# Performance work log

Hardware: AMD Instinct MI355X
Metric: run time of the kernel (lower is better)

Reference implementation:

```python
import jax, jax.numpy as jnp
import numpy as np

N, E, D = 50000, 800000, 64  # nodes, edges, hidden (in_hid == out_hid, n_heads == 1)


def setup_inputs() -> dict:
    key = jax.random.key(0)
    ks = jax.random.split(key, 12)

    def lin(k, out_d, in_d):
        k1, k2 = jax.random.split(k)
        s = 1.0 / np.sqrt(in_d)
        W = jax.random.uniform(k1, (out_d, in_d), minval=-s, maxval=s, dtype=jnp.float32)
        b = jax.random.uniform(k2, (out_d,), minval=-s, maxval=s, dtype=jnp.float32)
        return W, b

    Wt, bt = lin(ks[0], D, D + 1)   # w_transfer: Linear(d_input+1, d_k)
    Wq, bq = lin(ks[1], D, D)
    Wks, bks = lin(ks[2], D, D)
    Wkd, bkd = lin(ks[3], D, D)
    Wvs, bvs = lin(ks[4], D, D)
    Wvd, bvd = lin(ks[5], D, D)
    return {
        "x": jax.random.normal(ks[6], (N, D), dtype=jnp.float32),
        "edge_index": jax.random.randint(ks[7], (2, E), 0, N),
        "edge_time": jax.random.uniform(ks[8], (E,), dtype=jnp.float32),
        "x_time": jax.random.uniform(ks[9], (N,), dtype=jnp.float32),
        "edge_same": jax.random.randint(ks[10], (E,), 0, 2).astype(jnp.float32),
        "ln_gamma": jnp.ones((D,), jnp.float32),
        "ln_beta": jnp.zeros((D,), jnp.float32),
        "Wt": Wt, "bt": bt, "Wq": Wq, "bq": bq,
        "Wks": Wks, "bks": bks, "Wkd": Wkd, "bkd": bkd,
        "Wvs": Wvs, "bvs": bvs, "Wvd": Wvd, "bvd": bvd,
    }


def _gelu(x):
    return jax.nn.gelu(x, approximate=False)  # torch F.gelu default (erf)


def _temporal_enc(t):
    # TemporalEncoding: div_term[j] = 1/10000^(2*(j//2)/D); sin on even cols, cos on odd
    j = jnp.arange(D)
    div = 1.0 / jnp.power(jnp.float32(10000.0), (2.0 * (j // 2)).astype(jnp.float32) / D)
    pe = (t.reshape(-1, 1) * 200.0) * div[None, :]  # [E, D]
    return jnp.where((j % 2 == 0)[None, :], jnp.sin(pe), jnp.cos(pe))


def reference(x, edge_index, edge_time, x_time, edge_same, ln_gamma, ln_beta,
              Wt, bt, Wq, bq, Wks, bks, Wkd, bkd, Wvs, bvs, Wvd, bvd):
    residual = x
    # LayerNorm(d_input)
    mu = jnp.mean(x, axis=-1, keepdims=True)
    var = jnp.var(x, axis=-1, keepdims=True)
    xn = (x - mu) / jnp.sqrt(var + 1e-5) * ln_gamma + ln_beta

    src, dst = edge_index[0], edge_index[1]  # x_j = source, x_i = target (PyG default)
    x_j = xn[src]                            # [E, D] gather
    x_i = xn[dst]                            # [E, D] gather
    es = edge_same.reshape(-1, 1)            # [E, 1]

    te = _temporal_enc(edge_time)            # [E, D]
    xt = _gelu(jnp.concatenate([x_j, edge_time.reshape(-1, 1)], axis=1) @ Wt.T + bt) + te

    q = x_i @ Wq.T + bq
    k = es * (xt @ Wks.T + bks) + (1.0 - es) * (xt @ Wkd.T + bkd)
    att = jnp.sum(k * q, axis=-1) / jnp.sqrt(jnp.float32(D))  # [E]

    # PyG-style segment softmax over edges sharing the same receiver
    m = jax.ops.segment_max(att, dst, num_segments=N)
    m = jnp.where(jnp.isfinite(m), m, 0.0)
    ex = jnp.exp(att - m[dst])
    denom = jax.ops.segment_sum(ex, dst, num_segments=N)
    attn = ex / (denom[dst] + 1e-16)         # [E]

    v = es * (xt @ Wvs.T + bvs) + (1.0 - es) * (xt @ Wvd.T + bvd)
    aggr = jax.ops.segment_sum(attn[:, None] * v, dst, num_segments=N)  # [N, D]

    return residual + _gelu(aggr)            # dropout is identity in eval
```

## Files before the change

kernel.cpp:

```cpp
#include <hip/hip_runtime.h>
#include <hip/hip_bf16.h>
#include <math.h>

#define D 64

typedef __attribute__((ext_vector_type(8))) short bf16x8;
typedef __attribute__((ext_vector_type(8))) _Float16 f16x8;
typedef __attribute__((ext_vector_type(8))) unsigned short u16x8;
typedef __attribute__((ext_vector_type(4))) float f32x4;
typedef unsigned short u16;

__device__ __forceinline__ float gelu_erf(float x) {
    return 0.5f * x * (1.0f + erff(x * 0.70710678118654752f));
}
__device__ __forceinline__ float gelu_fast(float x) {
    float t = x * fmaf(x * x, -0.1029432f, -2.3022080f);
    float e = __builtin_amdgcn_exp2f(t);
    return x * __builtin_amdgcn_rcpf(1.0f + e);
}
__device__ __forceinline__ u16 f2bf(float v) {
    __hip_bfloat16 h = __float2bfloat16(v);
    return *(u16*)&h;
}
__device__ __forceinline__ float bf2f(u16 v) {
    return __uint_as_float(((unsigned int)v) << 16);
}
__device__ __forceinline__ u16 f2h(float v) {
    _Float16 h = (_Float16)v;
    return __builtin_bit_cast(u16, h);
}
__device__ __forceinline__ void atomic_pk_add_f16(u16* addr, float lo, float hi) {
    unsigned int p = (unsigned int)f2h(lo) | ((unsigned int)f2h(hi) << 16);
    asm volatile("global_atomic_pk_add_f16 %0, %1, off sc1" :: "v"(addr), "v"(p));
}
__device__ __forceinline__ int pi_perm(int p) { return ((p & 3) << 4) | (p >> 2); }

__device__ __forceinline__ float rowsum16(float v) {
    int x;
    x = __builtin_amdgcn_update_dpp(0, __builtin_bit_cast(int, v), 0xB1, 0xF, 0xF, true);
    v += __builtin_bit_cast(float, x);
    x = __builtin_amdgcn_update_dpp(0, __builtin_bit_cast(int, v), 0x4E, 0xF, 0xF, true);
    v += __builtin_bit_cast(float, x);
    x = __builtin_amdgcn_update_dpp(0, __builtin_bit_cast(int, v), 0x141, 0xF, 0xF, true);
    v += __builtin_bit_cast(float, x);
    x = __builtin_amdgcn_update_dpp(0, __builtin_bit_cast(int, v), 0x140, 0xF, 0xF, true);
    v += __builtin_bit_cast(float, x);
    return v;
}

__global__ __launch_bounds__(256) void prep_hist(
    const float* __restrict__ Wt, const float* __restrict__ Wq,
    const float* __restrict__ Wks, const float* __restrict__ Wkd,
    const float* __restrict__ Wvs, const float* __restrict__ Wvd,
    u16* __restrict__ WtB, u16* __restrict__ WqB,
    u16* __restrict__ WksB, u16* __restrict__ WkdB,
    u16* __restrict__ WvsB, u16* __restrict__ WvdB,
    const int* __restrict__ ei, const float* __restrict__ esame,
    int* __restrict__ cnt, int* __restrict__ rank, int E)
{
    if (blockIdx.x < 12) {
        int task = blockIdx.x * 4 + (threadIdx.x >> 6);
        int lane = threadIdx.x & 63;
        int wsel = task >> 3, f = task & 7;
        int c = lane & 15, quad = lane >> 4;
        int nt = f >> 1, kk = f & 1;
        for (int j = 0; j < 8; ++j) {
            int n = nt * 16 + c, k = kk * 32 + quad * 8 + j;
            float v; u16* dp; bool h16 = false;
            switch (wsel) {
                case 0: v = Wt[n * 65 + k];  dp = WtB;  break;
                case 1: v = Wq[n * 64 + k];  dp = WqB;  break;
                case 2: v = Wks[k * 64 + n]; dp = WksB; break;
                case 3: v = Wkd[k * 64 + n]; dp = WkdB; break;
                case 4: v = Wvs[n * 64 + pi_perm(k)]; dp = WvsB; h16 = true; break;
                default: v = Wvd[n * 64 + pi_perm(k)]; dp = WvdB; h16 = true; break;
            }
            dp[(f * 64 + lane) * 8 + j] = h16 ? f2h(v) : f2bf(v);
        }
    } else {
        int gid = (blockIdx.x - 12) * 256 + threadIdx.x;
        int stride = (gridDim.x - 12) * 256;
        int e[4]; bool v[4]; int key[4];
        #pragma unroll
        for (int j = 0; j < 4; ++j) { e[j] = gid + j * stride; v[j] = e[j] < E; }
        #pragma unroll
        for (int j = 0; j < 4; ++j) {
            if (v[j]) key[j] = 2 * ei[E + e[j]] + (esame[e[j]] > 0.5f ? 0 : 1);
        }
        int r[4];
        #pragma unroll
        for (int j = 0; j < 4; ++j) {
            if (v[j]) r[j] = atomicAdd(&cnt[key[j]], 1);
        }
        #pragma unroll
        for (int j = 0; j < 4; ++j) {
            if (v[j]) rank[e[j]] = r[j];
        }
    }
}

#define SCAN_CHUNK 2048

__global__ __launch_bounds__(256) void scan_phaseA(const int* __restrict__ cnt,
                                                   int* __restrict__ bsum, int M)
{
    int base = blockIdx.x * SCAN_CHUNK;
    int s = 0;
    for (int i = threadIdx.x; i < SCAN_CHUNK; i += 256) {
        int idx = base + i;
        s += (idx < M) ? cnt[idx] : 0;
    }
    #pragma unroll
    for (int o = 32; o; o >>= 1) s += __shfl_xor(s, o);
    __shared__ int red[4];
    if ((threadIdx.x & 63) == 0) red[threadIdx.x >> 6] = s;
    __syncthreads();
    if (threadIdx.x == 0) bsum[blockIdx.x] = red[0] + red[1] + red[2] + red[3];
}

__global__ __launch_bounds__(256) void scan_phaseC(const int* __restrict__ cnt,
                                                   const int* __restrict__ bsum,
                                                   int* __restrict__ cursor, int M)
{
    __shared__ int wsum[4];
    __shared__ int sboff;
    if (threadIdx.x < 64) {
        int v = ((int)threadIdx.x < (int)blockIdx.x) ? bsum[threadIdx.x] : 0;
        #pragma unroll
        for (int o = 32; o; o >>= 1) v += __shfl_xor(v, o);
        if (threadIdx.x == 0) sboff = v;
    }
    int base = blockIdx.x * SCAN_CHUNK;
    int i0 = base + threadIdx.x * 8;
    int vals[8];
    int tsum = 0;
    #pragma unroll
    for (int j = 0; j < 8; ++j) {
        int idx = i0 + j;
        vals[j] = (idx < M) ? cnt[idx] : 0;
        tsum += vals[j];
    }
    int lane = threadIdx.x & 63;
    int w = threadIdx.x >> 6;
    int inc = tsum;
    #pragma unroll
    for (int o = 1; o < 64; o <<= 1) {
        int v = __shfl_up(inc, o);
        if (lane >= o) inc += v;
    }
    if (lane == 63) wsum[w] = inc;
    __syncthreads();
    int woff = 0;
    #pragma unroll
    for (int k = 0; k < 4; ++k) woff += (k < w) ? wsum[k] : 0;
    int excl = woff + (inc - tsum) + sboff;
    #pragma unroll
    for (int j = 0; j < 8; ++j) {
        int idx = i0 + j;
        if (idx < M) cursor[idx] = excl;
        excl += vals[j];
    }
}

__global__ __launch_bounds__(256) void scatter_qgemm(
    const int* __restrict__ ei, const float* __restrict__ et,
    const float* __restrict__ esame, const int* __restrict__ cursor,
    const int* __restrict__ rank,
    int4* __restrict__ evk, int E, int GS,
    const float* __restrict__ x, const float* __restrict__ gamma, const float* __restrict__ beta,
    const u16* __restrict__ WqB, const u16* __restrict__ WksB, const u16* __restrict__ WkdB,
    const float* __restrict__ bq, const float* __restrict__ bks, const float* __restrict__ bkd,
    u16* __restrict__ xnb, u16* __restrict__ qk2, float* __restrict__ bq2, int N)
{
    __shared__ u16 qtile[4][16 * 64];
    __shared__ u16 stile[4][32 * 64];

    if (blockIdx.x < GS) {
        int gid = blockIdx.x * 256 + threadIdx.x;
        int stride = GS * 256;
        int e[4]; bool v[4]; int key[4]; int rk[4]; int src[4]; float tv[4];
        #pragma unroll
        for (int j = 0; j < 4; ++j) { e[j] = gid + j * stride; v[j] = e[j] < E; }
        #pragma unroll
        for (int j = 0; j < 4; ++j) {
            if (v[j]) {
                key[j] = 2 * ei[E + e[j]] + (esame[e[j]] > 0.5f ? 0 : 1);
                rk[j] = rank[e[j]];
                src[j] = ei[e[j]];
                tv[j] = et[e[j]];
            }
        }
        int pos[4];
        #pragma unroll
        for (int j = 0; j < 4; ++j) {
            if (v[j]) pos[j] = cursor[key[j]] + rk[j];
        }
        #pragma unroll
        for (int j = 0; j < 4; ++j) {
            if (v[j]) evk[pos[j]] = make_int4(key[j], __float_as_int(tv[j]), src[j], 0);
        }
        return;
    }

    const int lane = threadIdx.x & 63;
    const int c = lane & 15, quad = lane >> 4;
    const int w = threadIdx.x >> 6;
    const int wave = (blockIdx.x - GS) * 4 + w;
    const int n0r = wave * 16;
    const bool active = n0r < N;
    const int n0 = active ? n0r : 0;
    const int rowA = (n0 + c < N) ? n0 + c : N - 1;

    const float* xrow = x + (long)rowA * D;
    f32x4 xa = *(const f32x4*)(xrow + quad * 8);
    f32x4 xb = *(const f32x4*)(xrow + quad * 8 + 4);
    f32x4 xc = *(const f32x4*)(xrow + 32 + quad * 8);
    f32x4 xd = *(const f32x4*)(xrow + 32 + quad * 8 + 4);
    float s = 0.f, s2 = 0.f;
    #pragma unroll
    for (int j = 0; j < 4; ++j) {
        s += xa[j] + xb[j] + xc[j] + xd[j];
        s2 += xa[j] * xa[j] + xb[j] * xb[j] + xc[j] * xc[j] + xd[j] * xd[j];
    }
    s += __shfl_xor(s, 16);  s += __shfl_xor(s, 32);
    s2 += __shfl_xor(s2, 16); s2 += __shfl_xor(s2, 32);
    float mu = s * (1.0f / 64.0f);
    float var = s2 * (1.0f / 64.0f) - mu * mu;
    float rinv = rsqrtf(var + 1e-5f);
    f32x4 ga = *(const f32x4*)(gamma + quad * 8);
    f32x4 gb = *(const f32x4*)(gamma + quad * 8 + 4);
    f32x4 gc = *(const f32x4*)(gamma + 32 + quad * 8);
    f32x4 gd = *(const f32x4*)(gamma + 32 + quad * 8 + 4);
    f32x4 ba = *(const f32x4*)(beta + quad * 8);
    f32x4 bb = *(const f32x4*)(beta + quad * 8 + 4);
    f32x4 bc = *(const f32x4*)(beta + 32 + quad * 8);
    f32x4 bd = *(const f32x4*)(beta + 32 + quad * 8 + 4);
    bf16x8 a0, a1;
    #pragma unroll
    for (int j = 0; j < 4; ++j) {
        a0[j]     = (short)f2bf(fmaf((xa[j] - mu) * rinv, ga[j], ba[j]));
        a0[4 + j] = (short)f2bf(fmaf((xb[j] - mu) * rinv, gb[j], bb[j]));
        a1[j]     = (short)f2bf(fmaf((xc[j] - mu) * rinv, gc[j], bc[j]));
        a1[4 + j] = (short)f2bf(fmaf((xd[j] - mu) * rinv, gd[j], bd[j]));
    }
    *(bf16x8*)(xnb + (long)rowA * D + quad * 8) = a0;
    *(bf16x8*)(xnb + (long)rowA * D + 32 + quad * 8) = a1;

    float bqc[4], bksc[4], bkdc[4];
    #pragma unroll
    for (int t = 0; t < 4; ++t) {
        bqc[t] = bq[t * 16 + c]; bksc[t] = bks[t * 16 + c]; bkdc[t] = bkd[t * 16 + c];
    }

    f32x4 accq[4];
    #pragma unroll
    for (int t = 0; t < 4; ++t) {
        bf16x8 b0 = *(const bf16x8*)(WqB + ((t * 2 + 0) * 64 + lane) * 8);
        bf16x8 b1 = *(const bf16x8*)(WqB + ((t * 2 + 1) * 64 + lane) * 8);
        f32x4 z = {0.f, 0.f, 0.f, 0.f};
        z = __builtin_amdgcn_mfma_f32_16x16x32_bf16(a0, b0, z, 0, 0, 0);
        z = __builtin_amdgcn_mfma_f32_16x16x32_bf16(a1, b1, z, 0, 0, 0);
        accq[t] = z;
    }
    #pragma unroll
    for (int r = 0; r < 4; ++r) {
        float qv[4], ss = 0.f, sd = 0.f;
        #pragma unroll
        for (int t = 0; t < 4; ++t) {
            qv[t] = accq[t][r] + bqc[t];
            ss = fmaf(qv[t], bksc[t], ss);
            sd = fmaf(qv[t], bkdc[t], sd);
        }
        #pragma unroll
        for (int o = 1; o < 16; o <<= 1) { ss += __shfl_xor(ss, o); sd += __shfl_xor(sd, o); }
        int nrow = n0 + quad * 4 + r;
        if (active && c == 0 && nrow < N)
            *(float2*)(bq2 + 2 * nrow) = make_float2(ss, sd);
        #pragma unroll
        for (int t = 0; t < 4; ++t)
            qtile[w][(quad * 4 + r) * 64 + t * 16 + c] = f2bf(qv[t]);
    }
    __syncthreads();

    const u16* qrow = &qtile[w][c * 64 + quad * 8];
    bf16x8 q0 = *(const bf16x8*)(qrow);
    bf16x8 q1 = *(const bf16x8*)(qrow + 32);
    #pragma unroll
    for (int t = 0; t < 4; ++t) {
        bf16x8 bs0 = *(const bf16x8*)(WksB + ((t * 2 + 0) * 64 + lane) * 8);
        bf16x8 bs1 = *(const bf16x8*)(WksB + ((t * 2 + 1) * 64 + lane) * 8);
        bf16x8 bd0 = *(const bf16x8*)(WkdB + ((t * 2 + 0) * 64 + lane) * 8);
        bf16x8 bd1 = *(const bf16x8*)(WkdB + ((t * 2 + 1) * 64 + lane) * 8);
        f32x4 zs = {0.f, 0.f, 0.f, 0.f}, zd = {0.f, 0.f, 0.f, 0.f};
        zs = __builtin_amdgcn_mfma_f32_16x16x32_bf16(q0, bs0, zs, 0, 0, 0);
        zs = __builtin_amdgcn_mfma_f32_16x16x32_bf16(q1, bs1, zs, 0, 0, 0);
        zd = __builtin_amdgcn_mfma_f32_16x16x32_bf16(q0, bd0, zd, 0, 0, 0);
        zd = __builtin_amdgcn_mfma_f32_16x16x32_bf16(q1, bd1, zd, 0, 0, 0);
        #pragma unroll
        for (int r = 0; r < 4; ++r) {
            int m = quad * 4 + r;
            stile[w][(2 * m + 0) * 64 + c * 4 + t] = f2bf(zs[r]);
            stile[w][(2 * m + 1) * 64 + c * 4 + t] = f2bf(zd[r]);
        }
    }
    __syncthreads();
    if (active) {
        int nrows = min(16, N - n0);
        const u16x8* sp = (const u16x8*)&stile[w][0];
        u16x8* dp = (u16x8*)(qk2 + (long)(2 * n0) * D);
        int cnt8 = nrows * 16;
        for (int j = lane; j < cnt8; j += 64) dp[j] = sp[j];
    }
}

template<bool FULL>
__device__ __forceinline__ void edge_run(
    const int4* __restrict__ evk, const u16* __restrict__ xnb,
    const bf16x8* bfrag, const float* btc, const float* w64c,
    const float* dvr, float phr,
    const u16* __restrict__ qk2, const float* __restrict__ bq2,
    u16* __restrict__ A, float* __restrict__ den,
    int base, int end, int qchunk, int c, int quad)
{
    const float S = 0.18033688011f;
    int cur_key = -1;
    float racc0 = 0.f, racc1 = 0.f, racc2 = 0.f, racc3 = 0.f, rden = 0.f;
    ushort4 q4 = {0, 0, 0, 0};
    float bqv = 0.f;

    const int rowbase = base + (c >> 2) * qchunk + (c & 3);
    const int qbase   = base + quad * qchunk;
    const int last    = end - 1;

    int srcC = ((const int*)(evk + (FULL ? rowbase : min(rowbase, last))))[2];

    for (int i = 0; i < qchunk; i += 4) {
        const u16* ar = xnb + srcC * D + quad * 8;
        bf16x8 a0 = *(const bf16x8*)(ar);
        bf16x8 a1 = *(const bf16x8*)(ar + 32);

        srcC = ((const int*)(evk + min(rowbase + i + 4, last)))[2];

        int qb = qbase + i;
        int2 kt0 = *(const int2*)(evk + (FULL ? qb     : min(qb,     last)));
        int2 kt1 = *(const int2*)(evk + (FULL ? qb + 1 : min(qb + 1, last)));
        int2 kt2 = *(const int2*)(evk + (FULL ? qb + 2 : min(qb + 2, last)));
        int2 kt3 = *(const int2*)(evk + (FULL ? qb + 3 : min(qb + 3, last)));

        f32x4 acc[4];
        #pragma unroll
        for (int t = 0; t < 4; ++t) {
            f32x4 z = {0.f, 0.f, 0.f, 0.f};
            z = __builtin_amdgcn_mfma_f32_16x16x32_bf16(a0, bfrag[t * 2 + 0], z, 0, 0, 0);
            z = __builtin_amdgcn_mfma_f32_16x16x32_bf16(a1, bfrag[t * 2 + 1], z, 0, 0, 0);
            acc[t] = z;
        }

        #pragma unroll
        for (int r = 0; r < 4; ++r) {
            int2 kt = (r == 0) ? kt0 : (r == 1) ? kt1 : (r == 2) ? kt2 : kt3;
            int keym = kt.x;
            float tm = __int_as_float(kt.y);

            if (keym != cur_key) {
                ushort4 nq = *(const ushort4*)(qk2 + keym * D + c * 4);
                float nb = bq2[keym];
                if (cur_key >= 0) {
                    u16* ap = A + cur_key * D + c * 4;
                    atomic_pk_add_f16(ap, racc0, racc1);
                    atomic_pk_add_f16(ap + 2, racc2, racc3);
                    if (c == 0) atomicAdd(&den[cur_key], rden);
                }
                cur_key = keym;
                q4 = nq;
                bqv = nb * S;
                racc0 = racc1 = racc2 = racc3 = 0.f;
                rden = 0.f;
            }

            float x0 = acc[0][r] + fmaf(tm, w64c[0], btc[0]);
            float x1 = acc[1][r] + fmaf(tm, w64c[1], btc[1]);
            float x2 = acc[2][r] + fmaf(tm, w64c[2], btc[2]);
            float x3 = acc[3][r] + fmaf(tm, w64c[3], btc[3]);
            float v0 = gelu_fast(x0) + __builtin_amdgcn_sinf(fmaf(tm, dvr[0], phr));
            float v1 = gelu_fast(x1) + __builtin_amdgcn_sinf(fmaf(tm, dvr[1], phr));
            float v2 = gelu_fast(x2) + __builtin_amdgcn_sinf(fmaf(tm, dvr[2], phr));
            float v3 = gelu_fast(x3) + __builtin_amdgcn_sinf(fmaf(tm, dvr[3], phr));

            float p = v0 * bf2f(q4.x);
            p = fmaf(v1, bf2f(q4.y), p);
            p = fmaf(v2, bf2f(q4.z), p);
            p = fmaf(v3, bf2f(q4.w), p);
            p = rowsum16(p);

            float ex = __builtin_amdgcn_exp2f(fmaf(p, S, bqv));
            if (!FULL && (qbase + i + r >= end)) ex = 0.f;

            racc0 = fmaf(ex, v0, racc0);
            racc1 = fmaf(ex, v1, racc1);
            racc2 = fmaf(ex, v2, racc2);
            racc3 = fmaf(ex, v3, racc3);
            rden += ex;
        }
    }

    if (cur_key >= 0) {
        u16* ap = A + cur_key * D + c * 4;
        atomic_pk_add_f16(ap, racc0, racc1);
        atomic_pk_add_f16(ap + 2, racc2, racc3);
        if (c == 0) atomicAdd(&den[cur_key], rden);
    }
}

__global__ __launch_bounds__(256) void edge_pass(
    const int4* __restrict__ evk, const u16* __restrict__ xnb, const u16* __restrict__ WtB,
    const float* __restrict__ Wt, const float* __restrict__ bt,
    const u16* __restrict__ qk2, const float* __restrict__ bq2,
    u16* __restrict__ A, float* __restrict__ den, int E, int chunk)
{
    const int lane = threadIdx.x & 63;
    const int c = lane & 15, quad = lane >> 4;
    const int wave = blockIdx.x * 4 + (threadIdx.x >> 6);
    const int base = wave * chunk;
    if (base >= E) return;
    const int end = min(base + chunk, E);
    const int qchunk = chunk >> 2;

    bf16x8 bfrag[8];
    #pragma unroll
    for (int f = 0; f < 8; ++f)
        bfrag[f] = *(const bf16x8*)(WtB + (f * 64 + lane) * 8);

    float btc[4], w64c[4], dvr[4];
    #pragma unroll
    for (int t = 0; t < 4; ++t) {
        int dim = t * 16 + c;
        btc[t] = bt[dim];
        w64c[t] = Wt[dim * 65 + 64];
        dvr[t] = 31.830988618f * expf(-9.210340371976184f * (float)(2 * (dim >> 1)) * (1.0f / 64.0f));
    }
    const float phr = (c & 1) ? 0.25f : 0.0f;

    if (base + chunk <= E)
        edge_run<true>(evk, xnb, bfrag, btc, w64c, dvr, phr, qk2, bq2, A, den,
                       base, end, qchunk, c, quad);
    else
        edge_run<false>(evk, xnb, bfrag, btc, w64c, dvr, phr, qk2, bq2, A, den,
                        base, end, qchunk, c, quad);
}

__global__ __launch_bounds__(256) void vgemm(
    const float* __restrict__ x, const u16* __restrict__ A, const float* __restrict__ den,
    const u16* __restrict__ WvsB, const u16* __restrict__ WvdB,
    const float* __restrict__ bvs, const float* __restrict__ bvd,
    float* __restrict__ out, int N)
{
    const int lane = threadIdx.x & 63;
    const int c = lane & 15, quad = lane >> 4;
    const int wave = blockIdx.x * 4 + (threadIdx.x >> 6);
    const int n0 = wave * 16;
    if (n0 >= N) return;
    const int rowA = (n0 + c < N) ? n0 + c : N - 1;

    float bvsc[4], bvdc[4];
    #pragma unroll
    for (int t = 0; t < 4; ++t) { bvsc[t] = bvs[t * 16 + c]; bvdc[t] = bvd[t * 16 + c]; }

    const u16* srow = A + (long)(2 * rowA) * D + quad * 8;
    const u16* drow = A + (long)(2 * rowA + 1) * D + quad * 8;
    f16x8 s0 = *(const f16x8*)(srow);
    f16x8 s1 = *(const f16x8*)(srow + 32);
    f16x8 d0 = *(const f16x8*)(drow);
    f16x8 d1 = *(const f16x8*)(drow + 32);

    f32x4 oacc[4];
    #pragma unroll
    for (int t = 0; t < 4; ++t) {
        f16x8 bs0 = *(const f16x8*)(WvsB + ((t * 2 + 0) * 64 + lane) * 8);
        f16x8 bs1 = *(const f16x8*)(WvsB + ((t * 2 + 1) * 64 + lane) * 8);
        f16x8 bd0 = *(const f16x8*)(WvdB + ((t * 2 + 0) * 64 + lane) * 8);
        f16x8 bd1 = *(const f16x8*)(WvdB + ((t * 2 + 1) * 64 + lane) * 8);
        f32x4 z = {0.f, 0.f, 0.f, 0.f};
        z = __builtin_amdgcn_mfma_f32_16x16x32_f16(s0, bs0, z, 0, 0, 0);
        z = __builtin_amdgcn_mfma_f32_16x16x32_f16(s1, bs1, z, 0, 0, 0);
        z = __builtin_amdgcn_mfma_f32_16x16x32_f16(d0, bd0, z, 0, 0, 0);
        z = __builtin_amdgcn_mfma_f32_16x16x32_f16(d1, bd1, z, 0, 0, 0);
        oacc[t] = z;
    }

    #pragma unroll
    for (int r = 0; r < 4; ++r) {
        int n = n0 + quad * 4 + r;
        if (n >= N) continue;
        float ds = den[2 * n], dd = den[2 * n + 1];
        float inv = 1.0f / (ds + dd + 1e-16f);
        float fs = ds * inv, fd = dd * inv;
        #pragma unroll
        for (int t = 0; t < 4; ++t) {
            long idx = (long)n * D + t * 16 + c;
            float o = fmaf(oacc[t][r], inv, fmaf(fs, bvsc[t], fd * bvdc[t]));
            out[idx] = x[idx] + gelu_erf(o);
        }
    }
}

extern "C" void kernel_launch(void* const* d_in, const int* in_sizes, int n_in,
                              void* d_out, int out_size, void* d_ws, size_t ws_size,
                              hipStream_t stream) {
    const float* x        = (const float*)d_in[0];
    const int*   ei       = (const int*)d_in[1];
    const float* et       = (const float*)d_in[2];
    const float* esame    = (const float*)d_in[4];
    const float* ln_gamma = (const float*)d_in[5];
    const float* ln_beta  = (const float*)d_in[6];
    const float* Wt  = (const float*)d_in[7];
    const float* bt  = (const float*)d_in[8];
    const float* Wq  = (const float*)d_in[9];
    const float* bq  = (const float*)d_in[10];
    const float* Wks = (const float*)d_in[11];
    const float* bks = (const float*)d_in[12];
    const float* Wkd = (const float*)d_in[13];
    const float* bkd = (const float*)d_in[14];
    const float* Wvs = (const float*)d_in[15];
    const float* bvs = (const float*)d_in[16];
    const float* Wvd = (const float*)d_in[17];
    const float* bvd = (const float*)d_in[18];
    float* out = (float*)d_out;

    const int N = in_sizes[0] / D;
    const int E = in_sizes[2];
    const int M = 2 * N;

    u16* A      = (u16*)d_ws;
    float* den  = (float*)(A + (long)M * D);
    int* cnt    = (int*)(den + M);
    int* cursor = cnt + M;
    float* bq2  = (float*)(cursor + M);
    int4* evk   = (int4*)(bq2 + M);
    int* bsum   = (int*)(evk + E);
    u16* xnb    = (u16*)(bsum + 256);
    u16* qk2    = xnb + (long)N * D;
    u16* WtB    = qk2 + (long)M * D;
    u16* WqB    = WtB + 4096;
    u16* WksB   = WqB + 4096;
    u16* WkdB   = WksB + 4096;
    u16* WvsB   = WkdB + 4096;
    u16* WvdB   = WvsB + 4096;
    int* rank   = (int*)A;
    const size_t rankBytes = (size_t)E * 4;

    hipMemsetAsync((char*)A + rankBytes, 0,
                   ((size_t)M * D * 2 - rankBytes) + (size_t)M * 4 * 2, stream);

    const int GH = (E + 256 * 4 - 1) / (256 * 4);
    prep_hist<<<12 + GH, 256, 0, stream>>>(Wt, Wq, Wks, Wkd, Wvs, Wvd,
                                           WtB, WqB, WksB, WkdB, WvsB, WvdB,
                                           ei, esame, cnt, rank, E);
    const int nbScan = (M + SCAN_CHUNK - 1) / SCAN_CHUNK;
    scan_phaseA<<<nbScan, 256, 0, stream>>>(cnt, bsum, M);
    scan_phaseC<<<nbScan, 256, 0, stream>>>(cnt, bsum, cursor, M);

    const int GS = (E + 256 * 4 - 1) / (256 * 4);
    const int GQ = ((N + 15) / 16 + 3) / 4;
    scatter_qgemm<<<GS + GQ, 256, 0, stream>>>(
        ei, et, esame, cursor, rank, evk, E, GS,
        x, ln_gamma, ln_beta, WqB, WksB, WkdB, bq, bks, bkd,
        xnb, qk2, bq2, N);

    hipMemsetAsync(A, 0, rankBytes, stream);

    const int nwaves = 2048 * 4;
    const int chunk = ((E + nwaves * 16 - 1) / (nwaves * 16)) * 16;
    edge_pass<<<2048, 256, 0, stream>>>(evk, xnb, WtB, Wt, bt,
                                        qk2, bq2, A, den, E, chunk);
    vgemm<<<GQ, 256, 0, stream>>>(x, A, den, WvsB, WvdB, bvs, bvd, out, N);
}
```

Measured before the change: 236.2 us.

## Move Wt fragments to LDS, defer segment atomics, drop extra rank memset

The edge pass now stages the Wt bf16 fragments in shared memory and reads them from LDS on every iteration, where it previously kept them in registers. The goal is to free VGPRs and allow higher occupancy. Finished segment results are stashed as packed halves and flushed on the next iteration, so atomic latency overlaps with the MFMA and GELU work. The source-index prefetch is removed. When the workspace is large enough, rank gets its own buffer so the second memset launch is skipped. The cost is extra LDS reads per iteration and some stash bookkeeping.

Result: faster. 230.0 us (-2.6%).

```diff
diff --git a/kernel.cpp b/kernel.cpp
--- a/kernel.cpp
+++ b/kernel.cpp
@@ -29,9 +29,14 @@
     _Float16 h = (_Float16)v;
     return __builtin_bit_cast(u16, h);
 }
+__device__ __forceinline__ unsigned pk2h(float lo, float hi) {
+    return (unsigned)f2h(lo) | ((unsigned)f2h(hi) << 16);
+}
+__device__ __forceinline__ void atomic_pk_add_u32(u16* addr, unsigned p) {
+    asm volatile("global_atomic_pk_add_f16 %0, %1, off sc1" :: "v"(addr), "v"(p));
+}
 __device__ __forceinline__ void atomic_pk_add_f16(u16* addr, float lo, float hi) {
-    unsigned int p = (unsigned int)f2h(lo) | ((unsigned int)f2h(hi) << 16);
-    asm volatile("global_atomic_pk_add_f16 %0, %1, off sc1" :: "v"(addr), "v"(p));
+    atomic_pk_add_u32(addr, pk2h(lo, hi));
 }
 __device__ __forceinline__ int pi_perm(int p) { return ((p & 3) << 4) | (p >> 2); }
 
@@ -316,30 +321,32 @@
 template<bool FULL>
 __device__ __forceinline__ void edge_run(
     const int4* __restrict__ evk, const u16* __restrict__ xnb,
-    const bf16x8* bfrag, const float* btc, const float* w64c,
+    const u16* wfrag, const float* btc, const float* w64c,
     const float* dvr, float phr,
     const u16* __restrict__ qk2, const float* __restrict__ bq2,
     u16* __restrict__ A, float* __restrict__ den,
     int base, int end, int qchunk, int c, int quad)
 {
     const float S = 0.18033688011f;
+    const int lane = quad * 16 + c;
     int cur_key = -1;
     float racc0 = 0.f, racc1 = 0.f, racc2 = 0.f, racc3 = 0.f, rden = 0.f;
     ushort4 q4 = {0, 0, 0, 0};
     float bqv = 0.f;
+    int stash_key = -1; unsigned sp01 = 0, sp23 = 0; float srden = 0.f;
 
     const int rowbase = base + (c >> 2) * qchunk + (c & 3);
     const int qbase   = base + quad * qchunk;
     const int last    = end - 1;
 
-    int srcC = ((const int*)(evk + (FULL ? rowbase : min(rowbase, last))))[2];
-
     for (int i = 0; i < qchunk; i += 4) {
-        const u16* ar = xnb + srcC * D + quad * 8;
+        int eidx = rowbase + i;
+        int ec = FULL ? eidx : min(eidx, last);
+        int srcL = ((const int*)(evk + ec))[2];
+
+        const u16* ar = xnb + srcL * D + quad * 8;
         bf16x8 a0 = *(const bf16x8*)(ar);
         bf16x8 a1 = *(const bf16x8*)(ar + 32);
-
-        srcC = ((const int*)(evk + min(rowbase + i + 4, last)))[2];
 
         int qb = qbase + i;
         int2 kt0 = *(const int2*)(evk + (FULL ? qb     : min(qb,     last)));
@@ -347,12 +354,26 @@
         int2 kt2 = *(const int2*)(evk + (FULL ? qb + 2 : min(qb + 2, last)));
         int2 kt3 = *(const int2*)(evk + (FULL ? qb + 3 : min(qb + 3, last)));
 
+        if (stash_key >= 0) {
+            u16* ap = A + stash_key * D + c * 4;
+            atomic_pk_add_u32(ap, sp01);
+            atomic_pk_add_u32(ap + 2, sp23);
+            if (c == 0) atomicAdd(&den[stash_key], srden);
+            stash_key = -1;
+        }
+
+        unsigned woff = 0;
+        asm volatile("" : "+v"(woff));
+        const u16* wfx = wfrag + woff;
+
         f32x4 acc[4];
         #pragma unroll
         for (int t = 0; t < 4; ++t) {
+            bf16x8 b0 = *(const bf16x8*)(wfx + ((t * 2 + 0) * 64 + lane) * 8);
+            bf16x8 b1 = *(const bf16x8*)(wfx + ((t * 2 + 1) * 64 + lane) * 8);
             f32x4 z = {0.f, 0.f, 0.f, 0.f};
-            z = __builtin_amdgcn_mfma_f32_16x16x32_bf16(a0, bfrag[t * 2 + 0], z, 0, 0, 0);
-            z = __builtin_amdgcn_mfma_f32_16x16x32_bf16(a1, bfrag[t * 2 + 1], z, 0, 0, 0);
+            z = __builtin_amdgcn_mfma_f32_16x16x32_bf16(a0, b0, z, 0, 0, 0);
+            z = __builtin_amdgcn_mfma_f32_16x16x32_bf16(a1, b1, z, 0, 0, 0);
             acc[t] = z;
         }
 
@@ -361,22 +382,6 @@
             int2 kt = (r == 0) ? kt0 : (r == 1) ? kt1 : (r == 2) ? kt2 : kt3;
             int keym = kt.x;
             float tm = __int_as_float(kt.y);
-
-            if (keym != cur_key) {
-                ushort4 nq = *(const ushort4*)(qk2 + keym * D + c * 4);
-                float nb = bq2[keym];
-                if (cur_key >= 0) {
-                    u16* ap = A + cur_key * D + c * 4;
-                    atomic_pk_add_f16(ap, racc0, racc1);
-                    atomic_pk_add_f16(ap + 2, racc2, racc3);
-                    if (c == 0) atomicAdd(&den[cur_key], rden);
-                }
-                cur_key = keym;
-                q4 = nq;
-                bqv = nb * S;
-                racc0 = racc1 = racc2 = racc3 = 0.f;
-                rden = 0.f;
-            }
 
             float x0 = acc[0][r] + fmaf(tm, w64c[0], btc[0]);
             float x1 = acc[1][r] + fmaf(tm, w64c[1], btc[1]);
@@ -387,6 +392,28 @@
             float v2 = gelu_fast(x2) + __builtin_amdgcn_sinf(fmaf(tm, dvr[2], phr));
             float v3 = gelu_fast(x3) + __builtin_amdgcn_sinf(fmaf(tm, dvr[3], phr));
 
+            if (keym != cur_key) {
+                ushort4 nq = *(const ushort4*)(qk2 + keym * D + c * 4);
+                float nb = bq2[keym];
+                if (cur_key >= 0) {
+                    if (stash_key >= 0) {
+                        u16* ap = A + stash_key * D + c * 4;
+                        atomic_pk_add_u32(ap, sp01);
+                        atomic_pk_add_u32(ap + 2, sp23);
+                        if (c == 0) atomicAdd(&den[stash_key], srden);
+                    }
+                    sp01 = pk2h(racc0, racc1);
+                    sp23 = pk2h(racc2, racc3);
+                    srden = rden;
+                    stash_key = cur_key;
+                }
+                cur_key = keym;
+                q4 = nq;
+                bqv = nb * S;
+                racc0 = racc1 = racc2 = racc3 = 0.f;
+                rden = 0.f;
+            }
+
             float p = v0 * bf2f(q4.x);
             p = fmaf(v1, bf2f(q4.y), p);
             p = fmaf(v2, bf2f(q4.z), p);
@@ -404,6 +431,12 @@
         }
     }
 
+    if (stash_key >= 0) {
+        u16* ap = A + stash_key * D + c * 4;
+        atomic_pk_add_u32(ap, sp01);
+        atomic_pk_add_u32(ap + 2, sp23);
+        if (c == 0) atomicAdd(&den[stash_key], srden);
+    }
     if (cur_key >= 0) {
         u16* ap = A + cur_key * D + c * 4;
         atomic_pk_add_f16(ap, racc0, racc1);
@@ -418,6 +451,15 @@
     const u16* __restrict__ qk2, const float* __restrict__ bq2,
     u16* __restrict__ A, float* __restrict__ den, int E, int chunk)
 {
+    __shared__ u16 wfrag[4096];
+    {
+        u16x8* wf = (u16x8*)wfrag;
+        const u16x8* ws = (const u16x8*)WtB;
+        wf[threadIdx.x] = ws[threadIdx.x];
+        wf[threadIdx.x + 256] = ws[threadIdx.x + 256];
+    }
+    __syncthreads();
+
     const int lane = threadIdx.x & 63;
     const int c = lane & 15, quad = lane >> 4;
     const int wave = blockIdx.x * 4 + (threadIdx.x >> 6);
@@ -426,11 +468,6 @@
     const int end = min(base + chunk, E);
     const int qchunk = chunk >> 2;
 
-    bf16x8 bfrag[8];
-    #pragma unroll
-    for (int f = 0; f < 8; ++f)
-        bfrag[f] = *(const bf16x8*)(WtB + (f * 64 + lane) * 8);
-
     float btc[4], w64c[4], dvr[4];
     #pragma unroll
     for (int t = 0; t < 4; ++t) {
@@ -442,10 +479,10 @@
     const float phr = (c & 1) ? 0.25f : 0.0f;
 
     if (base + chunk <= E)
-        edge_run<true>(evk, xnb, bfrag, btc, w64c, dvr, phr, qk2, bq2, A, den,
+        edge_run<true>(evk, xnb, wfrag, btc, w64c, dvr, phr, qk2, bq2, A, den,
                        base, end, qchunk, c, quad);
     else
-        edge_run<false>(evk, xnb, bfrag, btc, w64c, dvr, phr, qk2, bq2, A, den,
+        edge_run<false>(evk, xnb, wfrag, btc, w64c, dvr, phr, qk2, bq2, A, den,
                         base, end, qchunk, c, quad);
 }
 
@@ -546,11 +583,19 @@
     u16* WkdB   = WksB + 4096;
     u16* WvsB   = WkdB + 4096;
     u16* WvdB   = WvsB + 4096;
-    int* rank   = (int*)A;
+
+    char* wsend = (char*)(WvdB + 4096);
+    const size_t usedBytes = (size_t)(wsend - (char*)d_ws);
     const size_t rankBytes = (size_t)E * 4;
-
-    hipMemsetAsync((char*)A + rankBytes, 0,
-                   ((size_t)M * D * 2 - rankBytes) + (size_t)M * 4 * 2, stream);
+    const bool rank_standalone = (ws_size >= usedBytes + rankBytes);
+    int* rank = rank_standalone ? (int*)wsend : (int*)A;
+
+    if (rank_standalone) {
+        hipMemsetAsync(A, 0, (size_t)M * D * 2 + (size_t)M * 4 * 2, stream);
+    } else {
+        hipMemsetAsync((char*)A + rankBytes, 0,
+                       ((size_t)M * D * 2 - rankBytes) + (size_t)M * 4 * 2, stream);
+    }
 
     const int GH = (E + 256 * 4 - 1) / (256 * 4);
     prep_hist<<<12 + GH, 256, 0, stream>>>(Wt, Wq, Wks, Wkd, Wvs, Wvd,
@@ -567,7 +612,8 @@
         x, ln_gamma, ln_beta, WqB, WksB, WkdB, bq, bks, bkd,
         xnb, qk2, bq2, N);
 
-    hipMemsetAsync(A, 0, rankBytes, stream);
+    if (!rank_standalone)
+        hipMemsetAsync(A, 0, rankBytes, stream);
 
     const int nwaves = 2048 * 4;
     const int chunk = ((E + nwaves * 16 - 1) / (nwaves * 16)) * 16;
```
